# Performance work log

Measured on AMD Instinct MI355X. Metric: run time of the kernel, lower is better.

The kernel has to match this reference:

```python
import jax, jax.numpy as jnp
import numpy as np

B, S, HID = 2, 2048, 4096
H, KV, D = 32, 8, 128  # query heads, kv heads, head_dim
ROPE_BASE = 10000.0


def apply_rope(x, cos, sin):
    # x: (B, h, S, D); cos/sin: (S, D) broadcast over (B, h)
    x1 = x[..., ::2]
    x2 = x[..., 1::2]
    rotated = jnp.stack((-x2, x1), axis=-1).reshape(x.shape)  # interleave back
    return x * cos + rotated * sin


def setup_inputs() -> dict:
    key = jax.random.key(0)
    ks = jax.random.split(key, 5)
    hidden_states = jax.random.normal(ks[0], (B, S, HID), jnp.float32)
    # real rotary tables (interleaved convention: each freq repeated twice)
    inv_freq = 1.0 / (ROPE_BASE ** (jnp.arange(0, D, 2, dtype=jnp.float32) / D))
    freqs = jnp.arange(S, dtype=jnp.float32)[:, None] * inv_freq  # (S, D/2)
    freqs = jnp.repeat(freqs, 2, axis=-1)  # (S, D)
    cos, sin = jnp.cos(freqs), jnp.sin(freqs)
    std = 0.02
    wq = jax.random.normal(ks[1], (H * D, HID), jnp.float32) * std
    wk = jax.random.normal(ks[2], (KV * D, HID), jnp.float32) * std
    wv = jax.random.normal(ks[3], (KV * D, HID), jnp.float32) * std
    wo = jax.random.normal(ks[4], (HID, H * D), jnp.float32) * std
    return {"hidden_states": hidden_states, "cos": cos, "sin": sin,
            "wq": wq, "wk": wk, "wv": wv, "wo": wo}


def reference(hidden_states, cos, sin, wq, wk, wv, wo):
    bsz, seq, _ = hidden_states.shape
    G = H // KV  # GQA group size
    q = (hidden_states @ wq.T).reshape(bsz, seq, H, D).transpose(0, 2, 1, 3)   # (B,H,S,D)
    k = (hidden_states @ wk.T).reshape(bsz, seq, KV, D).transpose(0, 2, 1, 3)  # (B,KV,S,D)
    v = (hidden_states @ wv.T).reshape(bsz, seq, KV, D).transpose(0, 2, 1, 3)
    q = apply_rope(q, cos, sin)
    k = apply_rope(k, cos, sin)
    # GQA without materializing repeated K/V: group query heads per KV head
    qg = q.reshape(bsz, KV, G, seq, D)
    scale = 1.0 / np.float32(np.sqrt(D))
    scores = jnp.einsum('bkgsd,bktd->bkgst', qg, k) * scale  # (B,KV,G,S,S)
    causal = jnp.tril(jnp.ones((seq, seq), bool))
    scores = jnp.where(causal, scores, jnp.finfo(scores.dtype).min)
    probs = jax.nn.softmax(scores, axis=-1)
    attn = jnp.einsum('bkgst,bktd->bkgsd', probs, v)  # (B,KV,G,S,D)
    attn = attn.reshape(bsz, H, seq, D).transpose(0, 2, 1, 3).reshape(bsz, seq, H * D)
    return attn @ wo.T
```

## Files before the change

### kernel.cpp

```cpp
#include <hip/hip_runtime.h>

typedef unsigned short u16;
typedef unsigned int u32;
using bf8 = __attribute__((ext_vector_type(8))) short;
using f4  = __attribute__((ext_vector_type(4))) float;

#define DEV __device__ __forceinline__

#define QSCALE (0.08838834764831845f * 1.4426950408889634f)

DEV u16 f2b(float f) {
  u32 u = __float_as_uint(f);
  u32 r = u + 0x7fff + ((u >> 16) & 1);
  return (u16)(r >> 16);
}
DEV u32 f2b_u(u32 u) {
  return (u + 0x7fff + ((u >> 16) & 1)) >> 16;
}
DEV float b2f(u32 bits) { return __uint_as_float(bits << 16); }

#define GLOAD16(g, l)                                                          \
  __builtin_amdgcn_global_load_lds((__attribute__((address_space(1))) u32*)(g),\
                                   (__attribute__((address_space(3))) u32*)(l),\
                                   16, 0, 0)

DEV f4 mfma16(bf8 a, bf8 b, f4 c) {
  return __builtin_amdgcn_mfma_f32_16x16x32_bf16(a, b, c, 0, 0, 0);
}

__global__ __launch_bounds__(256) void convert_kernel(
    const u16* __restrict__ src, u16* __restrict__ dst,
    const u32* __restrict__ probe, int n8) {
  const int t = blockIdx.x * 256 + threadIdx.x;
  if (t >= n8) return;
  const bool isf32 = (probe[0] == 0x3F800000u);
  const uint4* s4 = (const uint4*)src;
  uint4* d4 = (uint4*)dst;
  if (!isf32) {
    d4[t] = s4[t];
    return;
  }
  uint4 a = s4[2 * t];
  uint4 b = s4[2 * t + 1];
  uint4 o;
  o.x = f2b_u(a.x) | (f2b_u(a.y) << 16);
  o.y = f2b_u(a.z) | (f2b_u(a.w) << 16);
  o.z = f2b_u(b.x) | (f2b_u(b.y) << 16);
  o.w = f2b_u(b.z) | (f2b_u(b.w) << 16);
  d4[t] = o;
}

DEV void gemm_core(const u16* __restrict__ A, const u16* __restrict__ W,
                   int lda, int ldw, int K, int mb, int nb,
                   u16* As, u16* Bs, f4 (&acc)[4][4]) {
  const int tid = threadIdx.x;
  const int lane = tid & 63;
  const int wid = tid >> 6;
  const int l16 = lane & 15;
  const int quad = lane >> 4;
  const int wm = (wid >> 1) * 64;
  const int wn = (wid & 1) * 64;

  const int c0 = wid * 2;
  const int rowA0 = c0 * 16 + (lane >> 2);
  const int colb = (lane & 3) * 16;

  const char* gA = (const char*)(A + (size_t)(mb * 128 + rowA0) * lda) + colb;
  const char* gB = (const char*)(W + (size_t)(nb * 128 + rowA0) * ldw) + colb;
  char* lA = (char*)As + c0 * 1024;
  char* lB = (char*)Bs + c0 * 1024;
  const size_t strideA = (size_t)lda * 32;
  const size_t strideB = (size_t)ldw * 32;

  for (int k0 = 0; k0 < K; k0 += 32) {
    __syncthreads();
    GLOAD16(gA + (size_t)k0 * 2, lA);
    GLOAD16(gA + (size_t)k0 * 2 + strideA, lA + 1024);
    GLOAD16(gB + (size_t)k0 * 2, lB);
    GLOAD16(gB + (size_t)k0 * 2 + strideB, lB + 1024);
    __syncthreads();

    bf8 af[4], bw[4];
#pragma unroll
    for (int t = 0; t < 4; t++) {
      af[t] = *(const bf8*)(As + (wm + t * 16 + l16) * 32 + quad * 8);
      bw[t] = *(const bf8*)(Bs + (wn + t * 16 + l16) * 32 + quad * 8);
    }
#pragma unroll
    for (int mt = 0; mt < 4; mt++)
#pragma unroll
      for (int nt = 0; nt < 4; nt++)
        acc[mt][nt] = mfma16(af[mt], bw[nt], acc[mt][nt]);
  }
}

__global__ __launch_bounds__(256) void gemm_qkv_kernel(
    const u16* __restrict__ hidden, const u16* __restrict__ wq,
    const u16* __restrict__ wk, const u16* __restrict__ wv,
    u16* __restrict__ qo, u16* __restrict__ ko, u16* __restrict__ vto) {
  __shared__ u16 As[128 * 32];
  __shared__ u16 Bs[128 * 32];
  const int mb = blockIdx.x, yb = blockIdx.y;
  const u16* W;
  u16* C;
  int nb, ldc, mode;
  if (yb < 32)      { W = wq; C = qo;  nb = yb;      ldc = 4096; mode = 0; }
  else if (yb < 40) { W = wk; C = ko;  nb = yb - 32; ldc = 1024; mode = 0; }
  else              { W = wv; C = vto; nb = yb - 40; ldc = 0;    mode = 1; }

  f4 acc[4][4];
#pragma unroll
  for (int i = 0; i < 4; i++)
#pragma unroll
    for (int j = 0; j < 4; j++) acc[i][j] = (f4){0.f, 0.f, 0.f, 0.f};

  gemm_core(hidden, W, 4096, 4096, 4096, mb, nb, As, Bs, acc);

  const int tid = threadIdx.x, lane = tid & 63, wid = tid >> 6;
  const int l16 = lane & 15, quad = lane >> 4;
  const int wm = (wid >> 1) * 64, wn = (wid & 1) * 64;

  if (mode == 0) {
#pragma unroll
    for (int mt = 0; mt < 4; mt++)
#pragma unroll
      for (int nt = 0; nt < 4; nt++) {
        const int n = nb * 128 + wn + nt * 16 + l16;
        const int m0 = mb * 128 + wm + mt * 16 + quad * 4;
#pragma unroll
        for (int r = 0; r < 4; r++)
          C[(size_t)(m0 + r) * ldc + n] = f2b(acc[mt][nt][r]);
      }
  } else {
#pragma unroll
    for (int mt = 0; mt < 4; mt++)
#pragma unroll
      for (int nt = 0; nt < 4; nt++) {
        const int n = nb * 128 + wn + nt * 16 + l16;
        const int m0 = mb * 128 + wm + mt * 16 + quad * 4;
        const int b_ = m0 >> 11, s0 = m0 & 2047;
        ushort4 pk;
        pk.x = f2b(acc[mt][nt][0]);
        pk.y = f2b(acc[mt][nt][1]);
        pk.z = f2b(acc[mt][nt][2]);
        pk.w = f2b(acc[mt][nt][3]);
        *(ushort4*)(vto + ((size_t)(b_ * 1024 + n) << 11) + s0) = pk;
      }
  }
}

__global__ __launch_bounds__(256) void gemm_o_kernel(
    const u16* __restrict__ A, const u16* __restrict__ W,
    float* __restrict__ C) {
  __shared__ u16 As[128 * 32];
  __shared__ u16 Bs[128 * 32];
  const int mb = blockIdx.x, nb = blockIdx.y;
  f4 acc[4][4];
#pragma unroll
  for (int i = 0; i < 4; i++)
#pragma unroll
    for (int j = 0; j < 4; j++) acc[i][j] = (f4){0.f, 0.f, 0.f, 0.f};

  gemm_core(A, W, 4096, 4096, 4096, mb, nb, As, Bs, acc);

  const int tid = threadIdx.x, lane = tid & 63, wid = tid >> 6;
  const int l16 = lane & 15, quad = lane >> 4;
  const int wm = (wid >> 1) * 64, wn = (wid & 1) * 64;
#pragma unroll
  for (int mt = 0; mt < 4; mt++)
#pragma unroll
    for (int nt = 0; nt < 4; nt++) {
      const int n = nb * 128 + wn + nt * 16 + l16;
      const int m0 = mb * 128 + wm + mt * 16 + quad * 4;
#pragma unroll
      for (int r = 0; r < 4; r++)
        C[(size_t)(m0 + r) * 4096 + n] = acc[mt][nt][r];
    }
}

__global__ void rope_kernel(u16* __restrict__ x, const u16* __restrict__ cs,
                            const u16* __restrict__ sn, int shift, float scale,
                            int nthreads) {
  const int t = blockIdx.x * 256 + threadIdx.x;
  if (t >= nthreads) return;
  const size_t e = (size_t)t * 8;
  const int d = (int)(e & 127);
  const int s = (int)((e >> shift) & 2047);
  uint4 xv = *(const uint4*)(x + e);
  uint4 cv = *(const uint4*)(cs + (size_t)s * 128 + d);
  uint4 sv = *(const uint4*)(sn + (size_t)s * 128 + d);
  u32 xw[4] = {xv.x, xv.y, xv.z, xv.w};
  u32 cw[4] = {cv.x, cv.y, cv.z, cv.w};
  u32 sw[4] = {sv.x, sv.y, sv.z, sv.w};
  u32 ow[4];
#pragma unroll
  for (int i = 0; i < 4; i++) {
    float x0 = b2f(xw[i] & 0xffff), x1 = b2f(xw[i] >> 16);
    float c = b2f(cw[i] & 0xffff);
    float si = b2f(sw[i] & 0xffff);
    float o0 = (x0 * c - x1 * si) * scale;
    float o1 = (x1 * c + x0 * si) * scale;
    ow[i] = (u32)f2b(o0) | ((u32)f2b(o1) << 16);
  }
  uint4 ov = {ow[0], ow[1], ow[2], ow[3]};
  *(uint4*)(x + e) = ov;
}

__global__ __launch_bounds__(256) void attn_kernel(
    const u16* __restrict__ q, const u16* __restrict__ k,
    const u16* __restrict__ vt, u16* __restrict__ attn) {
  __shared__ u16 Ks[64 * 136];
  __shared__ u16 Vt[128 * 72];
  __shared__ u16 Ps[4][16 * 72];

  const int qblk = blockIdx.x, h = blockIdx.y, b = blockIdx.z;
  const int kv = h >> 2;
  const int tid = threadIdx.x, lane = tid & 63, wid = tid >> 6;
  const int l16 = lane & 15, quad = lane >> 4;

  const u16* qp =
      q + ((size_t)(b * 2048 + qblk * 64 + wid * 16 + l16) * 32 + h) * 128;
  bf8 aq[4];
#pragma unroll
  for (int ds = 0; ds < 4; ds++)
    aq[ds] = *(const bf8*)(qp + ds * 32 + quad * 8);

  f4 accO[8];
#pragma unroll
  for (int i = 0; i < 8; i++) accO[i] = (f4){0.f, 0.f, 0.f, 0.f};
  float mrow[4] = {-1e30f, -1e30f, -1e30f, -1e30f};
  float lrow[4] = {0.f, 0.f, 0.f, 0.f};

  const u16* kp = k + ((size_t)(b * 2048) * 8 + kv) * 128;
  const u16* vp = vt + (size_t)(b * 8 + kv) * 128 * 2048;

  const int qg = qblk * 64 + wid * 16 + quad * 4;

  for (int kt = 0; kt <= qblk; kt++) {
    const int key0 = kt * 64;
    __syncthreads();
#pragma unroll
    for (int rep = 0; rep < 4; rep++) {
      const int e = rep * 2048 + tid * 8;
      const int row = e >> 7, col = e & 127;
      *(uint4*)(Ks + row * 136 + col) =
          *(const uint4*)(kp + (size_t)(key0 + row) * 1024 + col);
    }
#pragma unroll
    for (int rep = 0; rep < 4; rep++) {
      const int e = rep * 2048 + tid * 8;
      const int row = e >> 6, col = e & 63;
      *(uint4*)(Vt + row * 72 + col) =
          *(const uint4*)(vp + (size_t)row * 2048 + key0 + col);
    }
    __syncthreads();

    f4 sc[4];
#pragma unroll
    for (int nt = 0; nt < 4; nt++) {
      sc[nt] = (f4){0.f, 0.f, 0.f, 0.f};
      const int krow = nt * 16 + l16;
#pragma unroll
      for (int ds = 0; ds < 4; ds++) {
        bf8 bk = *(const bf8*)(Ks + krow * 136 + ds * 32 + quad * 8);
        sc[nt] = mfma16(aq[ds], bk, sc[nt]);
      }
    }

    u16 pbits[4][4];
#pragma unroll
    for (int r = 0; r < 4; r++) {
      float mx = -1e30f;
#pragma unroll
      for (int nt = 0; nt < 4; nt++) {
        const int keyg = key0 + nt * 16 + l16;
        if (keyg > qg + r) sc[nt][r] = -1e30f;
        mx = fmaxf(mx, sc[nt][r]);
      }
#pragma unroll
      for (int off = 1; off < 16; off <<= 1)
        mx = fmaxf(mx, __shfl_xor(mx, off, 64));
      const float mn = fmaxf(mrow[r], mx);
      const float alpha = exp2f(mrow[r] - mn);
      mrow[r] = mn;
      float ps = 0.f;
#pragma unroll
      for (int nt = 0; nt < 4; nt++) {
        const float p = exp2f(sc[nt][r] - mn);
        ps += p;
        pbits[nt][r] = f2b(p);
      }
#pragma unroll
      for (int off = 1; off < 16; off <<= 1) ps += __shfl_xor(ps, off, 64);
      lrow[r] = lrow[r] * alpha + ps;
#pragma unroll
      for (int nt = 0; nt < 8; nt++) accO[nt][r] *= alpha;
    }

#pragma unroll
    for (int nt = 0; nt < 4; nt++)
#pragma unroll
      for (int r = 0; r < 4; r++)
        Ps[wid][(quad * 4 + r) * 72 + nt * 16 + l16] = pbits[nt][r];
    __syncthreads();

#pragma unroll
    for (int ks = 0; ks < 2; ks++) {
      bf8 ap = *(const bf8*)(&Ps[wid][l16 * 72 + ks * 32 + quad * 8]);
#pragma unroll
      for (int nt = 0; nt < 8; nt++) {
        bf8 bv = *(const bf8*)(Vt + (nt * 16 + l16) * 72 + ks * 32 + quad * 8);
        accO[nt] = mfma16(ap, bv, accO[nt]);
      }
    }
  }

  float inv[4];
#pragma unroll
  for (int r = 0; r < 4; r++) inv[r] = 1.0f / lrow[r];
#pragma unroll
  for (int nt = 0; nt < 8; nt++)
#pragma unroll
    for (int r = 0; r < 4; r++) {
      const int s = qblk * 64 + wid * 16 + quad * 4 + r;
      const int dcol = nt * 16 + l16;
      attn[((size_t)(b * 2048 + s) * 32 + h) * 128 + dcol] =
          f2b(accO[nt][r] * inv[r]);
    }
}

extern "C" void kernel_launch(void* const* d_in, const int* in_sizes, int n_in,
                              void* d_out, int out_size, void* d_ws,
                              size_t ws_size, hipStream_t stream) {
  const u16* hidden = (const u16*)d_in[0];
  const u16* cosp = (const u16*)d_in[1];
  const u16* sinp = (const u16*)d_in[2];
  const u16* wq = (const u16*)d_in[3];
  const u16* wk = (const u16*)d_in[4];
  const u16* wv = (const u16*)d_in[5];
  const u16* wo = (const u16*)d_in[6];
  const u32* probe = (const u32*)d_in[1];
  float* out = (float*)d_out;

  char* ws = (char*)d_ws;
  u16* hidden_n = (u16*)(ws);
  u16* attnb    = (u16*)(ws);
  u16* qb       = (u16*)(ws + 33554432);
  u16* kb       = (u16*)(ws + 67108864);
  u16* vtb      = (u16*)(ws + 75497472);
  u16* wq_n     = (u16*)(ws + 83886080);
  u16* wk_n     = (u16*)(ws + 117440512);
  u16* wv_n     = (u16*)(ws + 125829120);
  u16* wo_n     = (u16*)(ws + 134217728);
  u16* cos_n    = (u16*)(ws + 167772160);
  u16* sin_n    = (u16*)(ws + 168296448);

  dim3 blk(256);
  convert_kernel<<<dim3(8192), blk, 0, stream>>>(hidden, hidden_n, probe,
                                                 2097152);
  convert_kernel<<<dim3(8192), blk, 0, stream>>>(wq, wq_n, probe, 2097152);
  convert_kernel<<<dim3(2048), blk, 0, stream>>>(wk, wk_n, probe, 524288);
  convert_kernel<<<dim3(2048), blk, 0, stream>>>(wv, wv_n, probe, 524288);
  convert_kernel<<<dim3(8192), blk, 0, stream>>>(wo, wo_n, probe, 2097152);
  convert_kernel<<<dim3(128), blk, 0, stream>>>(cosp, cos_n, probe, 32768);
  convert_kernel<<<dim3(128), blk, 0, stream>>>(sinp, sin_n, probe, 32768);

  gemm_qkv_kernel<<<dim3(32, 48), blk, 0, stream>>>(hidden_n, wq_n, wk_n, wv_n,
                                                    qb, kb, vtb);
  rope_kernel<<<dim3(8192), blk, 0, stream>>>(qb, cos_n, sin_n, 12, QSCALE,
                                              2097152);
  rope_kernel<<<dim3(2048), blk, 0, stream>>>(kb, cos_n, sin_n, 10, 1.0f,
                                              524288);
  attn_kernel<<<dim3(32, 32, 2), blk, 0, stream>>>(qb, kb, vtb, attnb);
  gemm_o_kernel<<<dim3(32, 32), blk, 0, stream>>>(attnb, wo_n, out);
}
```

Measured before the change: 1.091 ms.

## Prefetch next K/V tile into registers and add lazy softmax rescaling

The attention loop now loads the next K/V tile into registers right after the LDS stores, so global loads overlap with the MFMA and softmax work of the current tile. The online softmax skips rescaling the accumulator unless the running max grows by more than a threshold of 8 (log2 units), which saves exp and multiply work. The barrier between writing P to LDS and reading it is removed because each wave only touches its own Ps slice. The price is more register pressure from holding the prefetched tiles, plus a relaxed max that could overflow if scores grow a lot.

```diff
diff --git a/kernel.cpp b/kernel.cpp
--- a/kernel.cpp
+++ b/kernel.cpp
@@ -236,24 +236,41 @@
 
   const int qg = qblk * 64 + wid * 16 + quad * 4;
 
+  int krow_[4], kcol_[4], vrow_[4], vcol_[4];
+#pragma unroll
+  for (int rep = 0; rep < 4; rep++) {
+    const int e = rep * 2048 + tid * 8;
+    krow_[rep] = e >> 7; kcol_[rep] = e & 127;
+    vrow_[rep] = e >> 6; vcol_[rep] = e & 63;
+  }
+
+  uint4 kreg[4], vreg[4];
+#pragma unroll
+  for (int rep = 0; rep < 4; rep++) {
+    kreg[rep] = *(const uint4*)(kp + (size_t)krow_[rep] * 1024 + kcol_[rep]);
+    vreg[rep] = *(const uint4*)(vp + (size_t)vrow_[rep] * 2048 + vcol_[rep]);
+  }
+
   for (int kt = 0; kt <= qblk; kt++) {
     const int key0 = kt * 64;
     __syncthreads();
 #pragma unroll
     for (int rep = 0; rep < 4; rep++) {
-      const int e = rep * 2048 + tid * 8;
-      const int row = e >> 7, col = e & 127;
-      *(uint4*)(Ks + row * 136 + col) =
-          *(const uint4*)(kp + (size_t)(key0 + row) * 1024 + col);
-    }
-#pragma unroll
-    for (int rep = 0; rep < 4; rep++) {
-      const int e = rep * 2048 + tid * 8;
-      const int row = e >> 6, col = e & 63;
-      *(uint4*)(Vt + row * 72 + col) =
-          *(const uint4*)(vp + (size_t)row * 2048 + key0 + col);
+      *(uint4*)(Ks + krow_[rep] * 136 + kcol_[rep]) = kreg[rep];
+      *(uint4*)(Vt + vrow_[rep] * 72 + vcol_[rep]) = vreg[rep];
     }
     __syncthreads();
+
+    if (kt < qblk) {
+      const int key1 = key0 + 64;
+#pragma unroll
+      for (int rep = 0; rep < 4; rep++) {
+        kreg[rep] =
+            *(const uint4*)(kp + (size_t)(key1 + krow_[rep]) * 1024 + kcol_[rep]);
+        vreg[rep] =
+            *(const uint4*)(vp + (size_t)vrow_[rep] * 2048 + key1 + vcol_[rep]);
+      }
+    }
 
     f4 sc[4];
 #pragma unroll
@@ -280,21 +297,25 @@
 #pragma unroll
       for (int off = 1; off < 16; off <<= 1)
         mx = fmaxf(mx, __shfl_xor(mx, off, 64));
-      const float mn = fmaxf(mrow[r], mx);
-      const float alpha = exp2f(mrow[r] - mn);
-      mrow[r] = mn;
+      if (mx - mrow[r] > 8.f) {
+        const float mn = fmaxf(mrow[r], mx);
+        const float alpha = exp2f(mrow[r] - mn);
+        mrow[r] = mn;
+        lrow[r] *= alpha;
+#pragma unroll
+        for (int nt = 0; nt < 8; nt++) accO[nt][r] *= alpha;
+      }
+      const float mr = mrow[r];
       float ps = 0.f;
 #pragma unroll
       for (int nt = 0; nt < 4; nt++) {
-        const float p = exp2f(sc[nt][r] - mn);
+        const float p = exp2f(sc[nt][r] - mr);
         ps += p;
         pbits[nt][r] = f2b(p);
       }
 #pragma unroll
       for (int off = 1; off < 16; off <<= 1) ps += __shfl_xor(ps, off, 64);
-      lrow[r] = lrow[r] * alpha + ps;
-#pragma unroll
-      for (int nt = 0; nt < 8; nt++) accO[nt][r] *= alpha;
+      lrow[r] += ps;
     }
 
 #pragma unroll
@@ -302,7 +323,6 @@
 #pragma unroll
       for (int r = 0; r < 4; r++)
         Ps[wid][(quad * 4 + r) * 72 + nt * 16 + l16] = pbits[nt][r];
-    __syncthreads();
 
 #pragma unroll
     for (int ks = 0; ks < 2; ks++) {
```

After: 1.377 ms. 1.26x slower.

## Load K/V MFMA fragments directly from global and use lazy softmax rescaling

Applied to the files above, without the earlier changes.

The attention kernel no longer stages K and V tiles through shared memory. Each lane loads its MFMA B-operand fragments straight from global memory, which removes both block-wide barriers per key tile and the barrier after the per-wave P store. Softmax rescaling now happens only when the running max grows by more than 8 in log2 units, skipping most accumulator rescales. The costs are redundant global/L2 traffic, since all four waves fetch the same K/V fragments, and a small risk to precision or overflow from the stale max threshold.

```diff
diff --git a/kernel.cpp b/kernel.cpp
--- a/kernel.cpp
+++ b/kernel.cpp
@@ -209,8 +209,6 @@
 __global__ __launch_bounds__(256) void attn_kernel(
     const u16* __restrict__ q, const u16* __restrict__ k,
     const u16* __restrict__ vt, u16* __restrict__ attn) {
-  __shared__ u16 Ks[64 * 136];
-  __shared__ u16 Vt[128 * 72];
   __shared__ u16 Ps[4][16 * 72];
 
   const int qblk = blockIdx.x, h = blockIdx.y, b = blockIdx.z;
@@ -231,38 +229,23 @@
   float mrow[4] = {-1e30f, -1e30f, -1e30f, -1e30f};
   float lrow[4] = {0.f, 0.f, 0.f, 0.f};
 
-  const u16* kp = k + ((size_t)(b * 2048) * 8 + kv) * 128;
-  const u16* vp = vt + (size_t)(b * 8 + kv) * 128 * 2048;
+  const u16* kfrag = k + ((size_t)(b * 2048 + l16) * 8 + kv) * 128 + quad * 8;
+  const u16* vfrag =
+      vt + ((size_t)(b * 8 + kv) * 128 + l16) * 2048 + quad * 8;
 
   const int qg = qblk * 64 + wid * 16 + quad * 4;
 
   for (int kt = 0; kt <= qblk; kt++) {
     const int key0 = kt * 64;
-    __syncthreads();
-#pragma unroll
-    for (int rep = 0; rep < 4; rep++) {
-      const int e = rep * 2048 + tid * 8;
-      const int row = e >> 7, col = e & 127;
-      *(uint4*)(Ks + row * 136 + col) =
-          *(const uint4*)(kp + (size_t)(key0 + row) * 1024 + col);
-    }
-#pragma unroll
-    for (int rep = 0; rep < 4; rep++) {
-      const int e = rep * 2048 + tid * 8;
-      const int row = e >> 6, col = e & 63;
-      *(uint4*)(Vt + row * 72 + col) =
-          *(const uint4*)(vp + (size_t)row * 2048 + key0 + col);
-    }
-    __syncthreads();
 
     f4 sc[4];
 #pragma unroll
     for (int nt = 0; nt < 4; nt++) {
       sc[nt] = (f4){0.f, 0.f, 0.f, 0.f};
-      const int krow = nt * 16 + l16;
 #pragma unroll
       for (int ds = 0; ds < 4; ds++) {
-        bf8 bk = *(const bf8*)(Ks + krow * 136 + ds * 32 + quad * 8);
+        bf8 bk = *(const bf8*)(kfrag + (size_t)(key0 + nt * 16) * 1024 +
+                               ds * 32);
         sc[nt] = mfma16(aq[ds], bk, sc[nt]);
       }
     }
@@ -280,21 +263,25 @@
 #pragma unroll
       for (int off = 1; off < 16; off <<= 1)
         mx = fmaxf(mx, __shfl_xor(mx, off, 64));
-      const float mn = fmaxf(mrow[r], mx);
-      const float alpha = exp2f(mrow[r] - mn);
-      mrow[r] = mn;
+      if (mx - mrow[r] > 8.f) {
+        const float mn = fmaxf(mrow[r], mx);
+        const float alpha = exp2f(mrow[r] - mn);
+        mrow[r] = mn;
+        lrow[r] *= alpha;
+#pragma unroll
+        for (int nt = 0; nt < 8; nt++) accO[nt][r] *= alpha;
+      }
+      const float mr = mrow[r];
       float ps = 0.f;
 #pragma unroll
       for (int nt = 0; nt < 4; nt++) {
-        const float p = exp2f(sc[nt][r] - mn);
+        const float p = exp2f(sc[nt][r] - mr);
         ps += p;
         pbits[nt][r] = f2b(p);
       }
 #pragma unroll
       for (int off = 1; off < 16; off <<= 1) ps += __shfl_xor(ps, off, 64);
-      lrow[r] = lrow[r] * alpha + ps;
-#pragma unroll
-      for (int nt = 0; nt < 8; nt++) accO[nt][r] *= alpha;
+      lrow[r] += ps;
     }
 
 #pragma unroll
@@ -302,14 +289,14 @@
 #pragma unroll
       for (int r = 0; r < 4; r++)
         Ps[wid][(quad * 4 + r) * 72 + nt * 16 + l16] = pbits[nt][r];
-    __syncthreads();
 
 #pragma unroll
     for (int ks = 0; ks < 2; ks++) {
       bf8 ap = *(const bf8*)(&Ps[wid][l16 * 72 + ks * 32 + quad * 8]);
 #pragma unroll
       for (int nt = 0; nt < 8; nt++) {
-        bf8 bv = *(const bf8*)(Vt + (nt * 16 + l16) * 72 + ks * 32 + quad * 8);
+        bf8 bv = *(const bf8*)(vfrag + (size_t)(nt * 16) * 2048 + key0 +
+                               ks * 32);
         accO[nt] = mfma16(ap, bv, accO[nt]);
       }
     }
```

Measured after the change: 1.657 ms. 51.9% more time.

## Transpose QK^T MFMA so softmax rows are lane-local, add lazy rescaling

Applied to the files above, without the earlier changes.

Swaps the MFMA operands so each lane holds scores for one query row. Row max and sum then need only two cross-quad shuffles instead of a 16-lane reduction per row. Adds lazy rescaling: the running max and output accumulators update only when the max grows by more than a threshold, and the causal mask is applied only on the diagonal tile. P is written to shared memory with packed 4-element stores, and the __syncthreads before the PV MMA is dropped because each wave uses its own Ps buffer. The risk is an unguarded P write/read across waves if the data layout assumptions are wrong, and lazy rescaling could overflow bf16 if the threshold is too loose.

```diff
diff --git a/kernel.cpp b/kernel.cpp
--- a/kernel.cpp
+++ b/kernel.cpp
@@ -228,13 +228,13 @@
   f4 accO[8];
 #pragma unroll
   for (int i = 0; i < 8; i++) accO[i] = (f4){0.f, 0.f, 0.f, 0.f};
-  float mrow[4] = {-1e30f, -1e30f, -1e30f, -1e30f};
-  float lrow[4] = {0.f, 0.f, 0.f, 0.f};
+  float m = -1e30f;
+  float l = 0.f;
 
   const u16* kp = k + ((size_t)(b * 2048) * 8 + kv) * 128;
   const u16* vp = vt + (size_t)(b * 8 + kv) * 128 * 2048;
 
-  const int qg = qblk * 64 + wid * 16 + quad * 4;
+  const int qglob = qblk * 64 + wid * 16 + l16;
 
   for (int kt = 0; kt <= qblk; kt++) {
     const int key0 = kt * 64;
@@ -263,46 +263,67 @@
 #pragma unroll
       for (int ds = 0; ds < 4; ds++) {
         bf8 bk = *(const bf8*)(Ks + krow * 136 + ds * 32 + quad * 8);
-        sc[nt] = mfma16(aq[ds], bk, sc[nt]);
+        sc[nt] = mfma16(bk, aq[ds], sc[nt]);
+      }
+    }
+
+    if (kt == qblk) {
+#pragma unroll
+      for (int nt = 0; nt < 4; nt++)
+#pragma unroll
+        for (int r = 0; r < 4; r++)
+          if (key0 + nt * 16 + quad * 4 + r > qglob) sc[nt][r] = -1e30f;
+    }
+
+    float mx = -1e30f;
+#pragma unroll
+    for (int nt = 0; nt < 4; nt++) {
+      const float a = fmaxf(fmaxf(sc[nt][0], sc[nt][1]),
+                            fmaxf(sc[nt][2], sc[nt][3]));
+      mx = fmaxf(mx, a);
+    }
+    mx = fmaxf(mx, __shfl_xor(mx, 16, 64));
+    mx = fmaxf(mx, __shfl_xor(mx, 32, 64));
+
+    const bool grow = (mx - m > 8.f);
+    float alpha = 1.f;
+    if (grow) {
+      alpha = exp2f(m - mx);
+      m = mx;
+      l *= alpha;
+    }
+    if (__ballot(grow)) {
+#pragma unroll
+      for (int r = 0; r < 4; r++) {
+        const float ar = __shfl(alpha, (lane & 48) | (quad * 4 + r), 64);
+#pragma unroll
+        for (int nt = 0; nt < 8; nt++) accO[nt][r] *= ar;
       }
     }
 
     u16 pbits[4][4];
-#pragma unroll
-    for (int r = 0; r < 4; r++) {
-      float mx = -1e30f;
-#pragma unroll
-      for (int nt = 0; nt < 4; nt++) {
-        const int keyg = key0 + nt * 16 + l16;
-        if (keyg > qg + r) sc[nt][r] = -1e30f;
-        mx = fmaxf(mx, sc[nt][r]);
-      }
-#pragma unroll
-      for (int off = 1; off < 16; off <<= 1)
-        mx = fmaxf(mx, __shfl_xor(mx, off, 64));
-      const float mn = fmaxf(mrow[r], mx);
-      const float alpha = exp2f(mrow[r] - mn);
-      mrow[r] = mn;
-      float ps = 0.f;
-#pragma unroll
-      for (int nt = 0; nt < 4; nt++) {
-        const float p = exp2f(sc[nt][r] - mn);
+    float ps = 0.f;
+#pragma unroll
+    for (int nt = 0; nt < 4; nt++)
+#pragma unroll
+      for (int r = 0; r < 4; r++) {
+        const float p = exp2f(sc[nt][r] - m);
         ps += p;
         pbits[nt][r] = f2b(p);
       }
-#pragma unroll
-      for (int off = 1; off < 16; off <<= 1) ps += __shfl_xor(ps, off, 64);
-      lrow[r] = lrow[r] * alpha + ps;
-#pragma unroll
-      for (int nt = 0; nt < 8; nt++) accO[nt][r] *= alpha;
-    }
-
-#pragma unroll
-    for (int nt = 0; nt < 4; nt++)
-#pragma unroll
-      for (int r = 0; r < 4; r++)
-        Ps[wid][(quad * 4 + r) * 72 + nt * 16 + l16] = pbits[nt][r];
-    __syncthreads();
+    ps += __shfl_xor(ps, 16, 64);
+    ps += __shfl_xor(ps, 32, 64);
+    l += ps;
+
+#pragma unroll
+    for (int nt = 0; nt < 4; nt++) {
+      ushort4 pk;
+      pk.x = pbits[nt][0];
+      pk.y = pbits[nt][1];
+      pk.z = pbits[nt][2];
+      pk.w = pbits[nt][3];
+      *(ushort4*)(&Ps[wid][l16 * 72 + nt * 16 + quad * 4]) = pk;
+    }
 
 #pragma unroll
     for (int ks = 0; ks < 2; ks++) {
@@ -315,9 +336,11 @@
     }
   }
 
+  const float invq = 1.0f / l;
   float inv[4];
 #pragma unroll
-  for (int r = 0; r < 4; r++) inv[r] = 1.0f / lrow[r];
+  for (int r = 0; r < 4; r++)
+    inv[r] = __shfl(invq, (lane & 48) | (quad * 4 + r), 64);
 #pragma unroll
   for (int nt = 0; nt < 8; nt++)
 #pragma unroll
```

After: 1.178 ms. 1.08x slower.
